# Kernel optimization log

Measured on AMD Instinct MI355X. Metric: run time of the kernel, lower is better.

Reference implementation:

```python
import jax, jax.numpy as jnp
import numpy as np

EPS = 1e-07
ALPHA = 1.0


def _bbox_iou_xywh(box1, box2, eps=EPS):
    # box1, box2: [N, 4] in (cx, cy, w, h) format
    x1, y1, w1, h1 = box1[:, 0], box1[:, 1], box1[:, 2], box1[:, 3]
    x2, y2, w2, h2 = box2[:, 0], box2[:, 1], box2[:, 2], box2[:, 3]
    b1_x1, b1_x2 = x1 - w1 / 2, x1 + w1 / 2
    b1_y1, b1_y2 = y1 - h1 / 2, y1 + h1 / 2
    b2_x1, b2_x2 = x2 - w2 / 2, x2 + w2 / 2
    b2_y1, b2_y2 = y2 - h2 / 2, y2 + h2 / 2
    inter_w = jnp.clip(jnp.minimum(b1_x2, b2_x2) - jnp.maximum(b1_x1, b2_x1), 0)
    inter_h = jnp.clip(jnp.minimum(b1_y2, b2_y2) - jnp.maximum(b1_y1, b2_y1), 0)
    inter = inter_w * inter_h
    union = w1 * h1 + w2 * h2 - inter + eps
    iou = inter / union
    # torch code: `iou if iou != 0 else iou + eps` applied per-box (1,1) tensor
    return jnp.where(iou == 0, iou + eps, iou)


def setup_inputs() -> dict:
    key = jax.random.key(0)
    k1, k2 = jax.random.split(key)
    N = 8388608
    preds = jax.random.uniform(k1, (N, 4), dtype=jnp.float32)
    gts = jax.random.uniform(k2, (N, 4), dtype=jnp.float32)
    return {"preds": preds, "gts": gts}


def reference(preds, gts):
    iou = _bbox_iou_xywh(preds, gts)          # [N]
    total = jnp.sum(jnp.log(iou))
    return -ALPHA * (total / preds.shape[0])  # scalar
```

## Files before the change

### kernel.cpp

```cpp
#include <hip/hip_runtime.h>

#define EPS 1e-7f

__global__ __launch_bounds__(256) void iou_partial_kernel(
    const float4* __restrict__ preds, const float4* __restrict__ gts,
    float* __restrict__ partial, int n) {
    int tid = blockIdx.x * blockDim.x + threadIdx.x;
    int stride = gridDim.x * blockDim.x;

    float acc = 0.0f;
    for (int i = tid; i < n; i += stride) {
        float4 p = preds[i];
        float4 g = gts[i];

        float hw1 = 0.5f * p.z, hh1 = 0.5f * p.w;
        float hw2 = 0.5f * g.z, hh2 = 0.5f * g.w;

        float b1x1 = p.x - hw1, b1x2 = p.x + hw1;
        float b1y1 = p.y - hh1, b1y2 = p.y + hh1;
        float b2x1 = g.x - hw2, b2x2 = g.x + hw2;
        float b2y1 = g.y - hh2, b2y2 = g.y + hh2;

        float iw = fmaxf(fminf(b1x2, b2x2) - fmaxf(b1x1, b2x1), 0.0f);
        float ih = fmaxf(fminf(b1y2, b2y2) - fmaxf(b1y1, b2y1), 0.0f);
        float inter = iw * ih;
        float uni = p.z * p.w + g.z * g.w - inter + EPS;
        float iou = inter / uni;
        iou = (iou == 0.0f) ? EPS : iou;
        acc += __logf(iou);
    }

    #pragma unroll
    for (int off = 32; off > 0; off >>= 1)
        acc += __shfl_down(acc, off, 64);

    __shared__ float s[4];
    int lane = threadIdx.x & 63;
    int wv = threadIdx.x >> 6;
    if (lane == 0) s[wv] = acc;
    __syncthreads();
    if (threadIdx.x == 0)
        partial[blockIdx.x] = s[0] + s[1] + s[2] + s[3];
}

__global__ __launch_bounds__(256) void iou_final_kernel(
    const float* __restrict__ partial, int nb, float* __restrict__ out, float inv_n) {
    double acc = 0.0;
    for (int i = threadIdx.x; i < nb; i += blockDim.x)
        acc += (double)partial[i];

    #pragma unroll
    for (int off = 32; off > 0; off >>= 1)
        acc += __shfl_down(acc, off, 64);

    __shared__ double s[4];
    int lane = threadIdx.x & 63;
    int wv = threadIdx.x >> 6;
    if (lane == 0) s[wv] = acc;
    __syncthreads();
    if (threadIdx.x == 0) {
        double total = s[0] + s[1] + s[2] + s[3];
        out[0] = (float)(-total * (double)inv_n);
    }
}

extern "C" void kernel_launch(void* const* d_in, const int* in_sizes, int n_in,
                              void* d_out, int out_size, void* d_ws, size_t ws_size,
                              hipStream_t stream) {
    const float4* preds = (const float4*)d_in[0];
    const float4* gts   = (const float4*)d_in[1];
    int n = in_sizes[0] / 4;

    float* partial = (float*)d_ws;
    float* out = (float*)d_out;

    const int BLOCKS = 2048;
    const int THREADS = 256;

    iou_partial_kernel<<<BLOCKS, THREADS, 0, stream>>>(preds, gts, partial, n);
    iou_final_kernel<<<1, THREADS, 0, stream>>>(partial, BLOCKS, out, 1.0f / (float)n);
}
```

Baseline: 48.87 us.

## Fuse final reduction via last-block atomic counter and unroll loads by four

```diff
diff --git a/kernel.cpp b/kernel.cpp
--- a/kernel.cpp
+++ b/kernel.cpp
@@ -2,66 +2,76 @@
 
 #define EPS 1e-7f
 
-__global__ __launch_bounds__(256) void iou_partial_kernel(
+__device__ __forceinline__ float iou_log(float4 p, float4 g) {
+    float hw1 = 0.5f * p.z, hh1 = 0.5f * p.w;
+    float hw2 = 0.5f * g.z, hh2 = 0.5f * g.w;
+    float iw = fmaxf(fminf(p.x + hw1, g.x + hw2) - fmaxf(p.x - hw1, g.x - hw2), 0.0f);
+    float ih = fmaxf(fminf(p.y + hh1, g.y + hh2) - fmaxf(p.y - hh1, g.y - hh2), 0.0f);
+    float inter = iw * ih;
+    float uni = p.z * p.w + g.z * g.w - inter + EPS;
+    float iou = inter / uni;
+    iou = (iou == 0.0f) ? EPS : iou;
+    return __logf(iou);
+}
+
+__global__ __launch_bounds__(256) void iou_fused_kernel(
     const float4* __restrict__ preds, const float4* __restrict__ gts,
-    float* __restrict__ partial, int n) {
-    int tid = blockIdx.x * blockDim.x + threadIdx.x;
-    int stride = gridDim.x * blockDim.x;
+    float* __restrict__ partial, unsigned int* __restrict__ counter,
+    float* __restrict__ out, int n, float inv_n, int nblocks) {
+    const int tid = blockIdx.x * blockDim.x + threadIdx.x;
+    const int stride = gridDim.x * blockDim.x;
 
     float acc = 0.0f;
-    for (int i = tid; i < n; i += stride) {
-        float4 p = preds[i];
-        float4 g = gts[i];
-
-        float hw1 = 0.5f * p.z, hh1 = 0.5f * p.w;
-        float hw2 = 0.5f * g.z, hh2 = 0.5f * g.w;
-
-        float b1x1 = p.x - hw1, b1x2 = p.x + hw1;
-        float b1y1 = p.y - hh1, b1y2 = p.y + hh1;
-        float b2x1 = g.x - hw2, b2x2 = g.x + hw2;
-        float b2y1 = g.y - hh2, b2y2 = g.y + hh2;
-
-        float iw = fmaxf(fminf(b1x2, b2x2) - fmaxf(b1x1, b2x1), 0.0f);
-        float ih = fmaxf(fminf(b1y2, b2y2) - fmaxf(b1y1, b2y1), 0.0f);
-        float inter = iw * ih;
-        float uni = p.z * p.w + g.z * g.w - inter + EPS;
-        float iou = inter / uni;
-        iou = (iou == 0.0f) ? EPS : iou;
-        acc += __logf(iou);
+    int i = tid;
+    for (; i + 3 * stride < n; i += 4 * stride) {
+        float4 p0 = preds[i];
+        float4 p1 = preds[i + stride];
+        float4 p2 = preds[i + 2 * stride];
+        float4 p3 = preds[i + 3 * stride];
+        float4 g0 = gts[i];
+        float4 g1 = gts[i + stride];
+        float4 g2 = gts[i + 2 * stride];
+        float4 g3 = gts[i + 3 * stride];
+        acc += iou_log(p0, g0);
+        acc += iou_log(p1, g1);
+        acc += iou_log(p2, g2);
+        acc += iou_log(p3, g3);
     }
+    for (; i < n; i += stride)
+        acc += iou_log(preds[i], gts[i]);
 
     #pragma unroll
     for (int off = 32; off > 0; off >>= 1)
         acc += __shfl_down(acc, off, 64);
 
     __shared__ float s[4];
-    int lane = threadIdx.x & 63;
-    int wv = threadIdx.x >> 6;
+    const int lane = threadIdx.x & 63;
+    const int wv = threadIdx.x >> 6;
     if (lane == 0) s[wv] = acc;
     __syncthreads();
-    if (threadIdx.x == 0)
+
+    __shared__ bool last;
+    if (threadIdx.x == 0) {
         partial[blockIdx.x] = s[0] + s[1] + s[2] + s[3];
-}
+        __threadfence();
+        unsigned int t = atomicAdd(counter, 1u);
+        last = (t == (unsigned int)(nblocks - 1));
+    }
+    __syncthreads();
+    if (!last) return;
 
-__global__ __launch_bounds__(256) void iou_final_kernel(
-    const float* __restrict__ partial, int nb, float* __restrict__ out, float inv_n) {
-    double acc = 0.0;
-    for (int i = threadIdx.x; i < nb; i += blockDim.x)
-        acc += (double)partial[i];
-
+    __threadfence();
+    double d = 0.0;
+    for (int j = threadIdx.x; j < nblocks; j += blockDim.x)
+        d += (double)partial[j];
     #pragma unroll
     for (int off = 32; off > 0; off >>= 1)
-        acc += __shfl_down(acc, off, 64);
-
-    __shared__ double s[4];
-    int lane = threadIdx.x & 63;
-    int wv = threadIdx.x >> 6;
-    if (lane == 0) s[wv] = acc;
+        d += __shfl_down(d, off, 64);
+    __shared__ double sd[4];
+    if (lane == 0) sd[wv] = d;
     __syncthreads();
-    if (threadIdx.x == 0) {
-        double total = s[0] + s[1] + s[2] + s[3];
-        out[0] = (float)(-total * (double)inv_n);
-    }
+    if (threadIdx.x == 0)
+        out[0] = (float)(-(sd[0] + sd[1] + sd[2] + sd[3]) * (double)inv_n);
 }
 
 extern "C" void kernel_launch(void* const* d_in, const int* in_sizes, int n_in,
@@ -71,12 +81,14 @@
     const float4* gts   = (const float4*)d_in[1];
     int n = in_sizes[0] / 4;
 
-    float* partial = (float*)d_ws;
-    float* out = (float*)d_out;
-
     const int BLOCKS = 2048;
     const int THREADS = 256;
 
-    iou_partial_kernel<<<BLOCKS, THREADS, 0, stream>>>(preds, gts, partial, n);
-    iou_final_kernel<<<1, THREADS, 0, stream>>>(partial, BLOCKS, out, 1.0f / (float)n);
+    float* partial = (float*)d_ws;
+    unsigned int* counter = (unsigned int*)((char*)d_ws + BLOCKS * sizeof(float));
+    float* out = (float*)d_out;
+
+    hipMemsetAsync(counter, 0, sizeof(unsigned int), stream);
+    iou_fused_kernel<<<BLOCKS, THREADS, 0, stream>>>(
+        preds, gts, partial, counter, out, n, 1.0f / (float)n, BLOCKS);
 }
```

New measurement: 113.8 us. 2.33x slower.
